# Optimization experiments

Measured on AMD Instinct MI355X. Metric: run time of the kernel, lower is better.

The kernel has to match this reference:

```python
import jax, jax.numpy as jnp
import numpy as np

N = 4096        # nodes
E = 131072      # edges (avg degree 32)
D = 128         # parser.d
H1, H2, H3 = 256, 128, 64   # parser.neurons_gnn
L = 2
THRESH = 0.6 ** L           # cosine-similarity cutoff used in attention()
SCALE = 0.05                # weight init scale


def setup_inputs() -> dict:
    key = jax.random.key(0)
    ks = jax.random.split(key, 14)
    X = jax.random.normal(ks[0], (N, D), dtype=jnp.float32)
    edge_index = jax.random.randint(ks[1], (2, E), 0, N, dtype=jnp.int64)
    W1 = jax.random.normal(ks[2], (D, H1), dtype=jnp.float32) * SCALE
    b1 = jnp.zeros((H1,), dtype=jnp.float32)
    a1w = jax.random.normal(ks[3], (2 * H1,), dtype=jnp.float32) * SCALE
    a1b = jnp.zeros((), dtype=jnp.float32)
    W2 = jax.random.normal(ks[4], (H1, H2), dtype=jnp.float32) * SCALE
    b2 = jnp.zeros((H2,), dtype=jnp.float32)
    a2w = jax.random.normal(ks[5], (2 * H2,), dtype=jnp.float32) * SCALE
    a2b = jnp.zeros((), dtype=jnp.float32)
    W3 = jax.random.normal(ks[6], (H2, H3), dtype=jnp.float32) * SCALE
    b3 = jnp.zeros((H3,), dtype=jnp.float32)
    return {"X": X, "edge_index": edge_index,
            "W1": W1, "b1": b1, "a1w": a1w, "a1b": a1b,
            "W2": W2, "b2": b2, "a2w": a2w, "a2b": a2b,
            "W3": W3, "b3": b3}


def _attention(h, src, dst, aw, ab):
    """Vectorized form of GNN.attention: edge-softmax neighbor aggregation
    plus dense cosine-thresholded all-pairs aggregation, averaged.
    attn_fc(cat(h_i, h_j)) = (h_i . aw_left) + (h_j . aw_right) + ab."""
    n, dh = h.shape
    al = h @ aw[:dh]            # [N] left half of attention projection
    ar = h @ aw[dh:]            # [N] right half
    # --- neighbor branch: a_ij = softmax-like normalized exp(leaky_relu(.)) over neighbors of i
    e = jnp.exp(jax.nn.leaky_relu(al[src] + ar[dst] + ab))   # [E]
    denom = jax.ops.segment_sum(e, src, num_segments=n)      # [N]
    a = e / denom[src]                                       # [E]
    h_a = h + jax.ops.segment_sum(a[:, None] * h[dst], src, num_segments=n)
    # --- dense branch: thresholded cosine similarity modulates attention score
    hn = h / jnp.linalg.norm(h, axis=1, keepdims=True)       # [N, dh]
    C = hn @ hn.T                                            # [N, N] cosine
    C = jnp.where(C <= THRESH, 0.0, C)
    S = al[:, None] + ar[None, :] + ab                       # [N, N] attn scores
    B = jnp.exp(C * jax.nn.leaky_relu(S))                    # [N, N]
    h1 = h + B @ h
    return 0.5 * (h_a + h1)


def reference(X, edge_index, W1, b1, a1w, a1b, W2, b2, a2w, a2b, W3, b3):
    src, dst = edge_index[0], edge_index[1]
    h = X @ W1 + b1
    h = _attention(h, src, dst, a1w, a1b)
    h = jax.nn.relu(h)
    h = h @ W2 + b2
    h = _attention(h, src, dst, a2w, a2b)
    h = jax.nn.relu(h)
    h = h @ W3 + b3
    # F.normalize(h, p=2, dim=1)
    h = h / jnp.maximum(jnp.linalg.norm(h, axis=1, keepdims=True), 1e-12)
    return h
```

## Files before the change

### kernel.cpp

```cpp
#include <hip/hip_runtime.h>
#include <math.h>

#define NN 4096
#define NE 131072

typedef short short8 __attribute__((ext_vector_type(8)));
typedef float f32x4 __attribute__((ext_vector_type(4)));
typedef unsigned short u16;

__device__ __forceinline__ float lrelu_f(float x) { return x > 0.0f ? x : 0.01f * x; }

__device__ __forceinline__ u16 f2bf(float x) {
  unsigned int u = __float_as_uint(x);
  unsigned int r = (u + 0x7FFF + ((u >> 16) & 1)) >> 16;
  return (u16)r;
}
__device__ __forceinline__ float bf2f(u16 b) { return __uint_as_float(((unsigned int)b) << 16); }

__device__ __forceinline__ void gload_lds16(const u16* g, u16* l) {
  __builtin_amdgcn_global_load_lds((const __attribute__((address_space(1))) void*)g,
                                   (__attribute__((address_space(3))) void*)l, 16, 0, 0);
}

__global__ __launch_bounds__(256) void wtrans_kernel(const float* __restrict__ W,
    u16* __restrict__ WThi, u16* __restrict__ WTlo, int K, int P) {
  __shared__ u16 th[32][33], tl[32][33];
  int bp = blockIdx.x, bk = blockIdx.y;
  int t = threadIdx.x, tx = t & 31, ty8 = t >> 5;
  #pragma unroll
  for (int r = 0; r < 4; ++r) {
    int k = bk * 32 + ty8 + r * 8;
    int p = bp * 32 + tx;
    float x = W[(size_t)k * P + p];
    u16 hi = f2bf(x);
    th[ty8 + r * 8][tx] = hi;
    tl[ty8 + r * 8][tx] = f2bf(x - bf2f(hi));
  }
  __syncthreads();
  #pragma unroll
  for (int r = 0; r < 4; ++r) {
    int p = bp * 32 + ty8 + r * 8;
    int k = bk * 32 + tx;
    WThi[(size_t)p * K + k] = th[tx][ty8 + r * 8];
    WTlo[(size_t)p * K + k] = tl[tx][ty8 + r * 8];
  }
}

template<bool RELU>
__global__ __launch_bounds__(256) void convert_io_kernel(const float* __restrict__ x,
    u16* __restrict__ ghi, u16* __restrict__ glo) {
  int idx = blockIdx.x * 256 + threadIdx.x;
  float v = x[idx];
  if (RELU) v = fmaxf(v, 0.0f);
  u16 hi = f2bf(v);
  ghi[idx] = hi;
  glo[idx] = f2bf(v - bf2f(hi));
}

template<int K, int P>
__global__ __launch_bounds__(256) void mgemm_kernel(
    const u16* __restrict__ Ahi, const u16* __restrict__ Alo,
    const u16* __restrict__ WThi, const u16* __restrict__ WTlo,
    const float* __restrict__ bias, float* __restrict__ O) {
  constexpr int KC = K / 32;
  int w = threadIdx.x >> 6, l = threadIdx.x & 63;
  int lr = l & 15, lk = l >> 4;
  int i0 = blockIdx.x * 16;
  int p0 = blockIdx.y * 64 + w * 16;
  const u16* arh = Ahi + (size_t)(i0 + lr) * K + lk * 8;
  const u16* arl = Alo + (size_t)(i0 + lr) * K + lk * 8;
  const u16* brh = WThi + (size_t)(p0 + lr) * K + lk * 8;
  const u16* brl = WTlo + (size_t)(p0 + lr) * K + lk * 8;
  f32x4 ahh = {0.f, 0.f, 0.f, 0.f};
  f32x4 ahl = {0.f, 0.f, 0.f, 0.f};
  f32x4 alh = {0.f, 0.f, 0.f, 0.f};
  #pragma unroll
  for (int c = 0; c < KC; ++c) {
    short8 Ah = *(const short8*)(arh + 32 * c);
    short8 Al = *(const short8*)(arl + 32 * c);
    short8 Bh = *(const short8*)(brh + 32 * c);
    short8 Bl = *(const short8*)(brl + 32 * c);
    ahh = __builtin_amdgcn_mfma_f32_16x16x32_bf16(Ah, Bh, ahh, 0, 0, 0);
    ahl = __builtin_amdgcn_mfma_f32_16x16x32_bf16(Ah, Bl, ahl, 0, 0, 0);
    alh = __builtin_amdgcn_mfma_f32_16x16x32_bf16(Al, Bh, alh, 0, 0, 0);
  }
  int p = p0 + lr;
  float bv = bias[p];
  #pragma unroll
  for (int q = 0; q < 4; ++q) {
    int i = i0 + 4 * lk + q;
    O[(size_t)i * P + p] = ahh[q] + ahl[q] + alh[q] + bv;
  }
}

template<int DH>
__global__ __launch_bounds__(256) void rowstats_kernel(const float* __restrict__ h,
    const float* __restrict__ aw, float* __restrict__ al, float* __restrict__ ar,
    float* __restrict__ inv) {
  constexpr int NC = DH / 64;
  int wid = threadIdx.x >> 6, lane = threadIdx.x & 63;
  int i = blockIdx.x * 4 + wid;
  float s2 = 0.f, sl = 0.f, sr = 0.f;
  #pragma unroll
  for (int c = 0; c < NC; ++c) {
    float x = h[(size_t)i * DH + c * 64 + lane];
    s2 = fmaf(x, x, s2);
    sl = fmaf(x, aw[c * 64 + lane], sl);
    sr = fmaf(x, aw[DH + c * 64 + lane], sr);
  }
  #pragma unroll
  for (int m = 32; m > 0; m >>= 1) {
    s2 += __shfl_xor(s2, m);
    sl += __shfl_xor(sl, m);
    sr += __shfl_xor(sr, m);
  }
  if (lane == 0) { al[i] = sl; ar[i] = sr; inv[i] = rsqrtf(s2); }
}

template<int DH>
__global__ void colsum_kernel(const float* __restrict__ h, float* __restrict__ cs) {
  int d = threadIdx.x;
  int r0 = blockIdx.x * (NN / 32);
  float s = 0.f;
  for (int i = 0; i < NN / 32; ++i) s += h[(size_t)(r0 + i) * DH + d];
  atomicAdd(&cs[d], s);
}

template<int DH>
__global__ __launch_bounds__(256) void convtrans_kernel(const float* __restrict__ h,
    u16* __restrict__ hhi, u16* __restrict__ hlo, u16* __restrict__ hT) {
  __shared__ u16 tile[32][33];
  int bx = blockIdx.x;
  int by = blockIdx.y;
  int t = threadIdx.x, tx = t & 31, ty8 = t >> 5;
  #pragma unroll
  for (int r = 0; r < 4; ++r) {
    int i = by * 32 + ty8 + r * 8;
    int d = bx * 32 + tx;
    float x = h[(size_t)i * DH + d];
    u16 hi = f2bf(x);
    hhi[(size_t)i * DH + d] = hi;
    hlo[(size_t)i * DH + d] = f2bf(x - bf2f(hi));
    tile[ty8 + r * 8][tx] = hi;
  }
  __syncthreads();
  #pragma unroll
  for (int r = 0; r < 4; ++r) {
    int d = bx * 32 + ty8 + r * 8;
    int i = by * 32 + tx;
    hT[(size_t)d * NN + i] = tile[tx][ty8 + r * 8];
  }
}

__global__ void hist_kernel(const int* __restrict__ src, int* __restrict__ counts) {
  int e = blockIdx.x * 256 + threadIdx.x;
  atomicAdd(&counts[src[e]], 1);
}

__global__ __launch_bounds__(1024) void scan_kernel(const int* __restrict__ counts,
    int* __restrict__ offsets, int* __restrict__ cursor) {
  __shared__ int part[1024];
  int t = threadIdx.x;
  int v[4]; int run = 0;
  #pragma unroll
  for (int j = 0; j < 4; ++j) { v[j] = counts[4 * t + j]; run += v[j]; }
  part[t] = run;
  __syncthreads();
  for (int off = 1; off < 1024; off <<= 1) {
    int y = (t >= off) ? part[t - off] : 0;
    __syncthreads();
    part[t] += y;
    __syncthreads();
  }
  int base = part[t] - run;
  #pragma unroll
  for (int j = 0; j < 4; ++j) { offsets[4 * t + j] = base; cursor[4 * t + j] = base; base += v[j]; }
  if (t == 1023) offsets[NN] = base;
}

__global__ void scatter_idx_kernel(const int* __restrict__ src, const int* __restrict__ dst,
    int* __restrict__ cursor, int* __restrict__ dstS) {
  int e = blockIdx.x * 256 + threadIdx.x;
  int s = src[e];
  int p = atomicAdd(&cursor[s], 1);
  dstS[p] = dst[e];
}

template<int DH>
__global__ __launch_bounds__(256) void gather_kernel(const float* __restrict__ h,
    const int* __restrict__ offsets, const int* __restrict__ dstS,
    const float* __restrict__ al, const float* __restrict__ ar,
    const float* __restrict__ ab, float* __restrict__ o) {
  constexpr int NC = DH / 64;
  int wid = threadIdx.x >> 6, lane = threadIdx.x & 63;
  int i = blockIdx.x * 4 + wid;
  int beg = offsets[i], end = offsets[i + 1];
  float base = al[i] + ab[0];
  float acc[NC] = {};
  float esum = 0.f;
  for (int k = beg; k < end; ++k) {
    int d = dstS[k];
    float e = expf(lrelu_f(base + ar[d]));
    esum += e;
    #pragma unroll
    for (int c = 0; c < NC; ++c)
      acc[c] = fmaf(e, h[(size_t)d * DH + c * 64 + lane], acc[c]);
  }
  float rd = (beg < end) ? 0.5f / esum : 0.0f;
  #pragma unroll
  for (int c = 0; c < NC; ++c)
    o[(size_t)i * DH + c * 64 + lane] = acc[c] * rd;
}

template<int DH>
__global__ __launch_bounds__(256) void qk_kernel(
    const u16* __restrict__ hhi, const u16* __restrict__ hlo,
    const float* __restrict__ al, const float* __restrict__ ar,
    const float* __restrict__ inv, const float* __restrict__ ab,
    u16* __restrict__ W, int* __restrict__ flags) {
  constexpr int KC = DH / 32;
  __shared__ u16 sA[2][2][128][32];
  __shared__ u16 sB[2][2][128][32];
  int i0 = blockIdx.x * 128;
  int j0 = blockIdx.y * 128;
  int w = threadIdx.x >> 6, l = threadIdx.x & 63;
  int wr = w >> 1, wc = w & 1;
  int lr = l & 15, lk = l >> 4;

  int rl = l >> 2;
  int sc = ((l & 3) ^ ((l >> 3) & 3)) * 8;
  const u16* gAh0 = hhi + (size_t)(i0 + 32 * w + rl) * DH + sc;
  const u16* gAl0 = hlo + (size_t)(i0 + 32 * w + rl) * DH + sc;
  const u16* gBh0 = hhi + (size_t)(j0 + 32 * w + rl) * DH + sc;
  const u16* gBl0 = hlo + (size_t)(j0 + 32 * w + rl) * DH + sc;

  f32x4 acc[4][4];
  #pragma unroll
  for (int q = 0; q < 4; ++q)
    #pragma unroll
    for (int s = 0; s < 4; ++s) acc[q][s] = (f32x4){0.f, 0.f, 0.f, 0.f};

#define QK_STAGE(buf, c) do { \
    gload_lds16(gAh0 + (c) * 32,           &sA[buf][0][32 * w][0]); \
    gload_lds16(gAh0 + 16 * DH + (c) * 32, &sA[buf][0][32 * w + 16][0]); \
    gload_lds16(gAl0 + (c) * 32,           &sA[buf][1][32 * w][0]); \
    gload_lds16(gAl0 + 16 * DH + (c) * 32, &sA[buf][1][32 * w + 16][0]); \
    gload_lds16(gBh0 + (c) * 32,           &sB[buf][0][32 * w][0]); \
    gload_lds16(gBh0 + 16 * DH + (c) * 32, &sB[buf][0][32 * w + 16][0]); \
    gload_lds16(gBl0 + (c) * 32,           &sB[buf][1][32 * w][0]); \
    gload_lds16(gBl0 + 16 * DH + (c) * 32, &sB[buf][1][32 * w + 16][0]); \
  } while (0)

  QK_STAGE(0, 0);
  __syncthreads();

  int cs = (lk ^ ((lr >> 1) & 3)) * 8;
  int cur = 0;
  for (int c = 0; c < KC; ++c) {
    if (c + 1 < KC) QK_STAGE(cur ^ 1, c + 1);
    short8 Ah[4], Al[4], Bh[4], Bl[4];
    #pragma unroll
    for (int q = 0; q < 4; ++q) {
      Ah[q] = *(const short8*)&sA[cur][0][64 * wr + 16 * q + lr][cs];
      Al[q] = *(const short8*)&sA[cur][1][64 * wr + 16 * q + lr][cs];
    }
    #pragma unroll
    for (int s = 0; s < 4; ++s) {
      Bh[s] = *(const short8*)&sB[cur][0][64 * wc + 16 * s + lr][cs];
      Bl[s] = *(const short8*)&sB[cur][1][64 * wc + 16 * s + lr][cs];
    }
    #pragma unroll
    for (int q = 0; q < 4; ++q)
      #pragma unroll
      for (int s = 0; s < 4; ++s) {
        acc[q][s] = __builtin_amdgcn_mfma_f32_16x16x32_bf16(Al[q], Bh[s], acc[q][s], 0, 0, 0);
        acc[q][s] = __builtin_amdgcn_mfma_f32_16x16x32_bf16(Ah[q], Bl[s], acc[q][s], 0, 0, 0);
        acc[q][s] = __builtin_amdgcn_mfma_f32_16x16x32_bf16(Ah[q], Bh[s], acc[q][s], 0, 0, 0);
      }
    __syncthreads();
    cur ^= 1;
  }
#undef QK_STAGE

  float abv = ab[0];
  int i_base = i0 + 64 * wr + 4 * lk;
  int j_base = j0 + 64 * wc + lr;
  float arj[4], invj[4];
  #pragma unroll
  for (int s = 0; s < 4; ++s) {
    int j = j_base + 16 * s;
    arj[s] = ar[j] + abv;
    invj[s] = inv[j];
  }
  int wany = 0;
  #pragma unroll
  for (int q = 0; q < 4; ++q) {
    float ali_[4], invi_[4];
    #pragma unroll
    for (int qq = 0; qq < 4; ++qq) {
      int i = i_base + 16 * q + qq;
      ali_[qq] = al[i];
      invi_[qq] = inv[i];
    }
    #pragma unroll
    for (int s = 0; s < 4; ++s)
      #pragma unroll
      for (int qq = 0; qq < 4; ++qq) {
        float C = acc[q][s][qq] * invi_[qq] * invj[s];
        float wv = 0.0f;
        if (C > 0.36f) wv = expm1f(C * lrelu_f(ali_[qq] + arj[s]));
        if (wv != 0.0f) wany = 1;
        W[(size_t)(i_base + 16 * q + qq) * NN + j_base + 16 * s] = f2bf(wv);
      }
  }
  int anyv = __any(wany) ? 1 : 0;
  if (l == 0)
    flags[((i0 >> 6) + wr) * 64 + (j0 >> 6) + wc] = anyv;
}

template<int DH>
__global__ __launch_bounds__(256) void pv_kernel(
    const u16* __restrict__ W, const u16* __restrict__ hT,
    const int* __restrict__ flags, const float* __restrict__ h,
    const float* __restrict__ cs, float* __restrict__ o) {
  __shared__ u16 sW[2][16][64];
  __shared__ u16 sT[2][4][16][64];
  __shared__ int list[64];
  __shared__ int nact_s;
  int ib = blockIdx.x;
  int w = threadIdx.x >> 6, l = threadIdx.x & 63;
  int lr = l & 15, lk = l >> 4;
  int i0 = ib * 16;
  int d0 = blockIdx.y * 64 + w * 16;
  const int* frow = flags + (i0 >> 6) * 64;
  if (threadIdx.x < 64) {
    int f = frow[threadIdx.x] != 0;
    unsigned long long m = __ballot(f);
    int pos = __popcll(m & ((1ULL << threadIdx.x) - 1ULL));
    if (f) list[pos] = threadIdx.x;
    if (threadIdx.x == 0) nact_s = __popcll(m);
  }
  __syncthreads();
  int nact = nact_s;

  int srow0 = l >> 3;
  int scol = ((l & 7) * 8) ^ ((srow0 & 7) << 3);
  const u16* gW0 = W + (size_t)(i0 + srow0) * NN + scol;
  const u16* gT0 = hT + (size_t)(d0 + srow0) * NN + scol;
  f32x4 acc0 = {0.f, 0.f, 0.f, 0.f};
  f32x4 acc1 = {0.f, 0.f, 0.f, 0.f};

  if (nact > 0) {
    {
      int j0 = list[0] * 64;
      if (w == 0) {
        gload_lds16(gW0 + j0, &sW[0][0][0]);
        gload_lds16(gW0 + 8 * NN + j0, &sW[0][8][0]);
      }
      gload_lds16(gT0 + j0, &sT[0][w][0][0]);
      gload_lds16(gT0 + 8 * NN + j0, &sT[0][w][8][0]);
    }
    __syncthreads();
    int cur = 0;
    for (int t = 0; t < nact; ++t) {
      if (t + 1 < nact) {
        int jn = list[t + 1] * 64;
        int nb = cur ^ 1;
        if (w == 0) {
          gload_lds16(gW0 + jn, &sW[nb][0][0]);
          gload_lds16(gW0 + 8 * NN + jn, &sW[nb][8][0]);
        }
        gload_lds16(gT0 + jn, &sT[nb][w][0][0]);
        gload_lds16(gT0 + 8 * NN + jn, &sT[nb][w][8][0]);
      }
      int sx = (lr & 7) << 3;
      short8 a0 = *(const short8*)&sW[cur][lr][(lk * 8) ^ sx];
      short8 a1 = *(const short8*)&sW[cur][lr][(32 + lk * 8) ^ sx];
      short8 b0 = *(const short8*)&sT[cur][w][lr][(lk * 8) ^ sx];
      short8 b1 = *(const short8*)&sT[cur][w][lr][(32 + lk * 8) ^ sx];
      acc0 = __builtin_amdgcn_mfma_f32_16x16x32_bf16(a0, b0, acc0, 0, 0, 0);
      acc1 = __builtin_amdgcn_mfma_f32_16x16x32_bf16(a1, b1, acc1, 0, 0, 0);
      __syncthreads();
      cur ^= 1;
    }
  }

  int d = d0 + lr;
  #pragma unroll
  for (int q = 0; q < 4; ++q) {
    int i = i0 + 4 * lk + q;
    size_t idx = (size_t)i * DH + d;
    o[idx] = o[idx] + h[idx] + 0.5f * cs[d] + 0.5f * (acc0[q] + acc1[q]);
  }
}

__global__ __launch_bounds__(256) void norm_kernel(float* __restrict__ out) {
  int wid = threadIdx.x >> 6, lane = threadIdx.x & 63;
  int i = blockIdx.x * 4 + wid;
  float x = out[(size_t)i * 64 + lane];
  float s = x * x;
  #pragma unroll
  for (int m = 32; m > 0; m >>= 1) s += __shfl_xor(s, m);
  float n = sqrtf(s);
  out[(size_t)i * 64 + lane] = x / fmaxf(n, 1e-12f);
}

struct Scratch {
  float *al, *ar, *inv, *cs;
  int *counts, *offsets, *cursor, *dstS, *flags;
  u16 *hhi, *hlo, *hT, *W;
  u16 *ghi, *glo, *wthi, *wtlo;
};

template<int DH>
static void run_attention(const float* h, const float* aw, const float* ab, float* o,
                          const Scratch& S, hipStream_t stream) {
  rowstats_kernel<DH><<<NN / 4, 256, 0, stream>>>(h, aw, S.al, S.ar, S.inv);
  hipMemsetAsync(S.cs, 0, DH * sizeof(float), stream);
  colsum_kernel<DH><<<32, DH, 0, stream>>>(h, S.cs);
  convtrans_kernel<DH><<<dim3(DH / 32, NN / 32), 256, 0, stream>>>(h, S.hhi, S.hlo, S.hT);
  gather_kernel<DH><<<NN / 4, 256, 0, stream>>>(h, S.offsets, S.dstS, S.al, S.ar, ab, o);
  qk_kernel<DH><<<dim3(NN / 128, NN / 128), 256, 0, stream>>>(
      S.hhi, S.hlo, S.al, S.ar, S.inv, ab, S.W, S.flags);
  pv_kernel<DH><<<dim3(NN / 16, DH / 64), 256, 0, stream>>>(
      S.W, S.hT, S.flags, h, S.cs, o);
}

extern "C" void kernel_launch(void* const* d_in, const int* in_sizes, int n_in,
                              void* d_out, int out_size, void* d_ws, size_t ws_size,
                              hipStream_t stream) {
  const float* X   = (const float*)d_in[0];
  const int*   ei  = (const int*)d_in[1];
  const float* W1  = (const float*)d_in[2];
  const float* b1  = (const float*)d_in[3];
  const float* a1w = (const float*)d_in[4];
  const float* a1b = (const float*)d_in[5];
  const float* W2  = (const float*)d_in[6];
  const float* b2  = (const float*)d_in[7];
  const float* a2w = (const float*)d_in[8];
  const float* a2b = (const float*)d_in[9];
  const float* W3  = (const float*)d_in[10];
  const float* b3  = (const float*)d_in[11];
  float* out = (float*)d_out;

  const int* src = ei;
  const int* dst = ei + NE;

  char* p = (char*)d_ws;
  auto alloc = [&](size_t bytes) { char* r = p; p += (bytes + 255) & ~(size_t)255; return r; };
  float* h1 = (float*)alloc((size_t)NN * 256 * 4);
  float* o1 = (float*)alloc((size_t)NN * 256 * 4);
  float* h2 = (float*)alloc((size_t)NN * 128 * 4);
  float* o2 = (float*)alloc((size_t)NN * 128 * 4);
  Scratch S;
  S.hhi = (u16*)alloc((size_t)NN * 256 * 2);
  S.hlo = (u16*)alloc((size_t)NN * 256 * 2);
  S.hT  = (u16*)alloc((size_t)NN * 256 * 2);
  S.W   = (u16*)alloc((size_t)NN * NN * 2);
  S.ghi = (u16*)alloc((size_t)NN * 256 * 2);
  S.glo = (u16*)alloc((size_t)NN * 256 * 2);
  S.wthi = (u16*)alloc((size_t)256 * 256 * 2);
  S.wtlo = (u16*)alloc((size_t)256 * 256 * 2);
  S.flags = (int*)alloc(4096 * 4);
  S.al    = (float*)alloc(NN * 4);
  S.ar    = (float*)alloc(NN * 4);
  S.inv   = (float*)alloc(NN * 4);
  S.cs    = (float*)alloc(256 * 4);
  S.counts  = (int*)alloc(NN * 4);
  S.offsets = (int*)alloc((NN + 1) * 4);
  S.cursor  = (int*)alloc(NN * 4);
  S.dstS    = (int*)alloc((size_t)NE * 4);

  hipMemsetAsync(S.counts, 0, NN * sizeof(int), stream);
  hist_kernel<<<NE / 256, 256, 0, stream>>>(src, S.counts);
  scan_kernel<<<1, 1024, 0, stream>>>(S.counts, S.offsets, S.cursor);
  scatter_idx_kernel<<<NE / 256, 256, 0, stream>>>(src, dst, S.cursor, S.dstS);

  wtrans_kernel<<<dim3(256 / 32, 128 / 32), 256, 0, stream>>>(W1, S.wthi, S.wtlo, 128, 256);
  convert_io_kernel<false><<<NN * 128 / 256, 256, 0, stream>>>(X, S.ghi, S.glo);
  mgemm_kernel<128, 256><<<dim3(NN / 16, 256 / 64), 256, 0, stream>>>(
      S.ghi, S.glo, S.wthi, S.wtlo, b1, h1);
  run_attention<256>(h1, a1w, a1b, o1, S, stream);

  wtrans_kernel<<<dim3(128 / 32, 256 / 32), 256, 0, stream>>>(W2, S.wthi, S.wtlo, 256, 128);
  convert_io_kernel<true><<<NN * 256 / 256, 256, 0, stream>>>(o1, S.ghi, S.glo);
  mgemm_kernel<256, 128><<<dim3(NN / 16, 128 / 64), 256, 0, stream>>>(
      S.ghi, S.glo, S.wthi, S.wtlo, b2, h2);
  run_attention<128>(h2, a2w, a2b, o2, S, stream);

  wtrans_kernel<<<dim3(64 / 32, 128 / 32), 256, 0, stream>>>(W3, S.wthi, S.wtlo, 128, 64);
  convert_io_kernel<true><<<NN * 128 / 256, 256, 0, stream>>>(o2, S.ghi, S.glo);
  mgemm_kernel<128, 64><<<dim3(NN / 16, 64 / 64), 256, 0, stream>>>(
      S.ghi, S.glo, S.wthi, S.wtlo, b3, out);
  norm_kernel<<<NN / 4, 256, 0, stream>>>(out);
}
```

Measured before the change: 277.5 us.

## Exploit cosine symmetry: compute upper-triangular QK tiles and write transposed weights

The QK kernel now skips tiles below the diagonal and, for each off-diagonal tile, computes both W[i,j] and W[j,i] from the shared symmetric cosine product. The transposed bf16 weights are staged through LDS with an XOR swizzle and stored as 16-byte vectors, and the matching block flags are set. This roughly halves the MFMA work of the dense similarity product, at the cost of a second exp per element, extra LDS traffic, a barrier, and half the launched blocks exiting immediately.

```diff
diff --git a/kernel.cpp b/kernel.cpp
--- a/kernel.cpp
+++ b/kernel.cpp
@@ -221,6 +221,8 @@
   constexpr int KC = DH / 32;
   __shared__ u16 sA[2][2][128][32];
   __shared__ u16 sB[2][2][128][32];
+  if (blockIdx.y < blockIdx.x) return;
+  const bool diag = (blockIdx.x == blockIdx.y);
   int i0 = blockIdx.x * 128;
   int j0 = blockIdx.y * 128;
   int w = threadIdx.x >> 6, l = threadIdx.x & 63;
@@ -285,37 +287,62 @@
   float abv = ab[0];
   int i_base = i0 + 64 * wr + 4 * lk;
   int j_base = j0 + 64 * wc + lr;
-  float arj[4], invj[4];
+  u16* tb = ((u16*)sA) + (size_t)w * 4096;
+  float arj[4], invj[4], alj[4];
   #pragma unroll
   for (int s = 0; s < 4; ++s) {
     int j = j_base + 16 * s;
     arj[s] = ar[j] + abv;
     invj[s] = inv[j];
-  }
-  int wany = 0;
+    alj[s] = al[j];
+  }
+  int wany = 0, wany_t = 0;
   #pragma unroll
   for (int q = 0; q < 4; ++q) {
-    float ali_[4], invi_[4];
+    float ali_[4], invi_[4], ari_[4];
     #pragma unroll
     for (int qq = 0; qq < 4; ++qq) {
       int i = i_base + 16 * q + qq;
       ali_[qq] = al[i];
       invi_[qq] = inv[i];
+      ari_[qq] = ar[i] + abv;
     }
     #pragma unroll
     for (int s = 0; s < 4; ++s)
       #pragma unroll
       for (int qq = 0; qq < 4; ++qq) {
         float C = acc[q][s][qq] * invi_[qq] * invj[s];
-        float wv = 0.0f;
-        if (C > 0.36f) wv = expm1f(C * lrelu_f(ali_[qq] + arj[s]));
+        float wv = 0.0f, wt = 0.0f;
+        if (C > 0.36f) {
+          wv = expm1f(C * lrelu_f(ali_[qq] + arj[s]));
+          if (!diag) wt = expm1f(C * lrelu_f(alj[s] + ari_[qq]));
+        }
         if (wv != 0.0f) wany = 1;
+        if (wt != 0.0f) wany_t = 1;
         W[(size_t)(i_base + 16 * q + qq) * NN + j_base + 16 * s] = f2bf(wv);
+        if (!diag) {
+          int rt = 16 * s + lr;
+          int ct = 16 * q + 4 * lk + qq;
+          tb[rt * 64 + (ct ^ ((rt & 7) << 3))] = f2bf(wt);
+        }
       }
   }
   int anyv = __any(wany) ? 1 : 0;
   if (l == 0)
     flags[((i0 >> 6) + wr) * 64 + (j0 >> 6) + wc] = anyv;
+  if (!diag) {
+    int anyt = __any(wany_t) ? 1 : 0;
+    __syncthreads();
+    #pragma unroll
+    for (int it = 0; it < 8; ++it) {
+      int row = it * 8 + (l >> 3);
+      int ch = (l & 7) * 8;
+      short8 v = *(const short8*)&tb[row * 64 + (ch ^ ((row & 7) << 3))];
+      *(short8*)&W[(size_t)(j0 + 64 * wc + row) * NN + i0 + 64 * wr + ch] = v;
+    }
+    if (l == 0)
+      flags[((j0 >> 6) + wc) * 64 + (i0 >> 6) + wr] = anyt;
+  }
 }
 
 template<int DH>
```

New measurement: 359.2 us. 1.29x slower.
